# Performance work log

Hardware: AMD Instinct MI355X
Metric: run time of the kernel (lower is better)

## Reference

```python
import jax, jax.numpy as jnp
import numpy as np

N_NODES = 100000
N_EDGES = 1600000
IN_C = 128
HID_C = 128
OUT_C = 64
N_GRAPHS = 64


def setup_inputs() -> dict:
    key = jax.random.key(0)
    ks = jax.random.split(key, 12)
    x = jax.random.normal(ks[0], (N_NODES, IN_C), dtype=jnp.float32)
    edge_index = jax.random.randint(ks[1], (2, N_EDGES), 0, N_NODES, dtype=jnp.int64)
    batch = jnp.sort(jax.random.randint(ks[2], (N_NODES,), 0, N_GRAPHS, dtype=jnp.int64))
    def glorot(k, fan_in, fan_out):
        s = jnp.sqrt(6.0 / (fan_in + fan_out))
        return jax.random.uniform(k, (fan_in, fan_out), jnp.float32, -s, s)
    W1 = glorot(ks[3], IN_C, HID_C);  b1 = jnp.zeros((HID_C,), jnp.float32)
    W2 = glorot(ks[4], HID_C, HID_C); b2 = jnp.zeros((HID_C,), jnp.float32)
    W3 = glorot(ks[5], HID_C, HID_C); b3 = jnp.zeros((HID_C,), jnp.float32)
    Wlin = glorot(ks[6], HID_C, OUT_C)
    blin = jnp.zeros((OUT_C,), jnp.float32)
    return {"x": x, "edge_index": edge_index, "batch": batch,
            "W1": W1, "b1": b1, "W2": W2, "b2": b2, "W3": W3, "b3": b3,
            "Wlin": Wlin, "blin": blin}


def _gcn_conv(x, W, b, src, dst, norm):
    # PyG GCNConv: h = x @ W; out[dst] += norm * h[src]; out += b
    h = x @ W
    msg = h[src] * norm[:, None]                     # [E+N, C] edge-wise gather (memory-bound)
    out = jax.ops.segment_sum(msg, dst, num_segments=N_NODES)
    return out + b


def reference(x, edge_index, batch, W1, b1, W2, b2, W3, b3, Wlin, blin):
    # add self-loops (PyG default add_self_loops=True)
    loops = jnp.arange(N_NODES, dtype=edge_index.dtype)
    src = jnp.concatenate([edge_index[0], loops])
    dst = jnp.concatenate([edge_index[1], loops])
    # symmetric normalization: deg over dst with unit edge weights
    deg = jax.ops.segment_sum(jnp.ones_like(src, dtype=x.dtype), dst, num_segments=N_NODES)
    dinv = jnp.where(deg > 0, jax.lax.rsqrt(deg), 0.0)
    norm = dinv[src] * dinv[dst]                     # [E+N]

    h = jax.nn.relu(_gcn_conv(x, W1, b1, src, dst, norm))
    h = jax.nn.relu(_gcn_conv(h, W2, b2, src, dst, norm))
    h = jax.nn.relu(_gcn_conv(h, W3, b3, src, dst, norm))

    # global mean pool over graphs
    sums = jax.ops.segment_sum(h, batch, num_segments=N_GRAPHS)
    cnts = jax.ops.segment_sum(jnp.ones((N_NODES,), h.dtype), batch, num_segments=N_GRAPHS)
    pooled = sums / jnp.clip(cnts, 1.0)[:, None]     # [G, HID_C]
    return pooled @ Wlin + blin                      # [G, OUT_C]
```

## Files before the change

### kernel.cpp

```cpp
#include <hip/hip_runtime.h>
#include <stdint.h>

#define C_HID 128
#define NGRAPH 64
#define COUT 64
#define POOL_S 64
#define NBLK 256
#define BKT 256
#define NBUK_MAX 512
#define SCAN_CH 4096

typedef short bf16x8 __attribute__((ext_vector_type(8)));
typedef float f32x4 __attribute__((ext_vector_type(4)));
typedef float f32x2 __attribute__((ext_vector_type(2)));

__device__ __forceinline__ unsigned short f2bf(float f){
  unsigned int u = __builtin_bit_cast(unsigned int, f);
  u = u + 0x7FFFu + ((u >> 16) & 1u);
  return (unsigned short)(u >> 16);
}
__device__ __forceinline__ float bflo(unsigned int u){
  return __builtin_bit_cast(float, u << 16);
}
__device__ __forceinline__ float bfhi(unsigned int u){
  return __builtin_bit_cast(float, u & 0xFFFF0000u);
}
__device__ __forceinline__ int clampi(int v, int lo, int hi){
  return v < lo ? lo : (v > hi ? hi : v);
}

__global__ void k_zero(float* __restrict__ out, int n){
  int i = blockIdx.x*blockDim.x + threadIdx.x;
  if (i < n) out[i] = 0.f;
}

__global__ __launch_bounds__(256) void k_cnt(const int* __restrict__ dst,
                                             int* __restrict__ cntg,
                                             int E, int N, int NBUK, int chunk){
  __shared__ int cnt[NBUK_MAX];
  int blk = blockIdx.x, t = threadIdx.x;
  for (int b = t; b < NBUK; b += 256) cnt[b] = 0;
  __syncthreads();
  int e0 = blk*chunk, e1 = min(E, e0 + chunk);
  for (int e = e0 + t; e < e1; e += 256)
    atomicAdd(&cnt[clampi(dst[e], 0, N-1) >> 8], 1);
  __syncthreads();
  for (int b = t; b < NBUK; b += 256)
    cntg[b*NBLK + blk] = cnt[b];
}

__global__ __launch_bounds__(256) void k_scanA(const int* __restrict__ cnt,
                                               int* __restrict__ bsum, int n){
  __shared__ int red[256];
  int blk = blockIdx.x, t = threadIdx.x;
  int base = blk*SCAN_CH + t*16;
  int s = 0;
  #pragma unroll
  for (int j = 0; j < 16; ++j){ int i = base + j; s += (i < n) ? cnt[i] : 0; }
  red[t] = s; __syncthreads();
  for (int off = 128; off > 0; off >>= 1){
    if (t < off) red[t] += red[t + off];
    __syncthreads();
  }
  if (t == 0) bsum[blk] = red[0];
}

__global__ __launch_bounds__(256) void k_scanB(const int* __restrict__ bsum,
                                               int* __restrict__ bbase,
                                               int* __restrict__ bases, int nb, int n){
  __shared__ int buf[256];
  int t = threadIdx.x;
  int v = (t < nb) ? bsum[t] : 0;
  buf[t] = v; __syncthreads();
  for (int off = 1; off < 256; off <<= 1){
    int add = (t >= off) ? buf[t-off] : 0;
    __syncthreads();
    buf[t] += add;
    __syncthreads();
  }
  if (t < nb) bbase[t] = buf[t] - v;
  if (t == nb-1) bases[n] = buf[t];
}

__global__ __launch_bounds__(256) void k_scanC(const int* __restrict__ cnt,
                                               const int* __restrict__ bbase,
                                               int* __restrict__ bases, int n){
  __shared__ int buf[256];
  int blk = blockIdx.x, t = threadIdx.x;
  int base = blk*SCAN_CH + t*16;
  int loc[16]; int s = 0;
  #pragma unroll
  for (int j = 0; j < 16; ++j){ int i = base + j; loc[j] = (i < n) ? cnt[i] : 0; s += loc[j]; }
  buf[t] = s; __syncthreads();
  for (int off = 1; off < 256; off <<= 1){
    int add = (t >= off) ? buf[t-off] : 0;
    __syncthreads();
    buf[t] += add;
    __syncthreads();
  }
  int run = bbase[blk] + buf[t] - s;
  #pragma unroll
  for (int j = 0; j < 16; ++j){
    int i = base + j;
    if (i < n) bases[i] = run;
    run += loc[j];
  }
}

__global__ __launch_bounds__(256) void k_scat(const int* __restrict__ src,
                                              const int* __restrict__ dst,
                                              const int* __restrict__ bases,
                                              unsigned int* __restrict__ rec,
                                              int E, int N, int NBUK, int chunk){
  __shared__ int cur[NBUK_MAX];
  int blk = blockIdx.x, t = threadIdx.x;
  for (int b = t; b < NBUK; b += 256) cur[b] = bases[b*NBLK + blk];
  __syncthreads();
  int e0 = blk*chunk, e1 = min(E, e0 + chunk);
  for (int e = e0 + t; e < e1; e += 256){
    int d = clampi(dst[e], 0, N-1);
    int s = clampi(src[e], 0, N-1);
    int p = atomicAdd(&cur[d >> 8], 1);
    rec[p] = (unsigned int)s | ((unsigned int)(d & 255) << 24);
  }
}

__global__ __launch_bounds__(256) void k_csr(const unsigned int* __restrict__ rec,
                                             const int* __restrict__ bases,
                                             int* __restrict__ offs, float* __restrict__ dinv,
                                             int* __restrict__ meta, int E, int N, int NBUK){
  __shared__ int cnt[BKT], loff[BKT], cur[BKT];
  int b = blockIdx.x, t = threadIdx.x;
  cnt[t] = 0;
  __syncthreads();
  int r0 = bases[b*NBLK];
  int r1 = (b+1 < NBUK) ? bases[(b+1)*NBLK] : E;
  for (int i = r0 + t; i < r1; i += 256)
    atomicAdd(&cnt[rec[i] >> 24], 1);
  __syncthreads();
  loff[t] = cnt[t];
  __syncthreads();
  for (int off = 1; off < BKT; off <<= 1){
    int add = (t >= off) ? loff[t - off] : 0;
    __syncthreads();
    loff[t] += add;
    __syncthreads();
  }
  int excl = loff[t] - cnt[t];
  cur[t] = r0 + excl;
  int node = b*BKT + t;
  if (node < N){
    offs[node] = r0 + excl;
    dinv[node] = rsqrtf((float)(cnt[t] + 1));
  }
  if (b == NBUK-1 && t == 0) offs[N] = E;
  __syncthreads();
  for (int i = r0 + t; i < r1; i += 256){
    unsigned int r = rec[i];
    int p = atomicAdd(&cur[r >> 24], 1);
    meta[p] = (int)(r & 0x00FFFFFFu);
  }
}

__global__ void k_xcast(const float2* __restrict__ x, const float* __restrict__ dinv,
                        unsigned short* __restrict__ y, unsigned short* __restrict__ y2, int N){
  int i = blockIdx.x*256 + threadIdx.x;
  int tot = N*64;
  if (i < tot){
    float2 v = x[i];
    float dn = dinv[i >> 6] * 64.f;
    int p = __builtin_amdgcn_cvt_pk_fp8_f32(v.x*dn, v.y*dn, 0, false);
    y[i] = (unsigned short)(p & 0xFFFF);
  } else if (i < tot + 64){
    y[i] = 0;
    y2[i] = 0;
  }
}

__global__ void k_prep(const float* __restrict__ W1, const float* __restrict__ W2,
                       const float* __restrict__ W3, unsigned short* __restrict__ Wt){
  int idx = blockIdx.x*256 + threadIdx.x;
  int w = idx >> 14;
  int r = idx & 16383;
  int n = r & 127, k = r >> 7;
  const float* W = (w == 0) ? W1 : (w == 1) ? W2 : W3;
  Wt[(size_t)w*16384 + (size_t)n*128 + k] = f2bf(W[k*128 + n]);
}

__global__ void k_spmm(const unsigned short* __restrict__ y, const int* __restrict__ offs,
                       const float* __restrict__ dinv, const int* __restrict__ meta,
                       unsigned int* __restrict__ agg, int N){
  int wv   = __builtin_amdgcn_readfirstlane(threadIdx.x >> 6);
  int lane = threadIdx.x & 63;
  int node = blockIdx.x*4 + wv;
  if (node >= N) return;
  int e0 = offs[node], e1 = offs[node+1];
  int cnt = e1 - e0;
  const int* mrow = meta + e0;

  float ax, ay;
  { f32x2 f = __builtin_amdgcn_cvt_pk_f32_fp8((int)y[(size_t)node*64 + lane], false);
    ax = f.x; ay = f.y; }

  for (int e = 0; e < cnt; e += 8){
    int s[8]; unsigned short u[8];
    #pragma unroll
    for (int j = 0; j < 8; ++j){
      int ij = e + j;
      int sj = mrow[ij];
      s[j] = (ij < cnt) ? sj : N;
    }
    #pragma unroll
    for (int j = 0; j < 8; ++j)
      u[j] = y[(size_t)s[j]*64 + lane];
    #pragma unroll
    for (int j = 0; j < 8; ++j){
      f32x2 f = __builtin_amdgcn_cvt_pk_f32_fp8((int)u[j], false);
      ax += f.x;
      ay += f.y;
    }
  }
  float dn = dinv[node] * 0.015625f;
  ax *= dn; ay *= dn;
  agg[(size_t)node*64 + lane] = (unsigned int)f2bf(ax) | ((unsigned int)f2bf(ay) << 16);
}

#define GEMM_BLOCKS 512
template<bool FP8OUT>
__global__ __launch_bounds__(256) void k_gemm(const unsigned short* __restrict__ A,
                                              const unsigned short* __restrict__ Wt,
                                              const float* __restrict__ bias,
                                              const float* __restrict__ scale,
                                              void* __restrict__ outv, int M){
  __shared__ unsigned short wt[128*136];
  {
    const uint4* wsrc = (const uint4*)Wt;
    for (int i = threadIdx.x; i < 4096; i += 256){
      uint4 v = wsrc[i];
      int n = i >> 4, kblk = i & 15;
      *(uint4*)&wt[n*136 + kblk*8] = v;
    }
  }
  __syncthreads();

  int wv = threadIdx.x >> 6, lane = threadIdx.x & 63;
  int q = lane >> 4, ln = lane & 15;
  int tiles = (M + 63) >> 6;

  for (int tile = blockIdx.x; tile < tiles; tile += GEMM_BLOCKS){
    int m0 = tile*64 + wv*16;
    int arow = m0 + ln;
    bool arow_ok = (arow < M);
    int arow_s = arow_ok ? arow : 0;

    f32x4 zero = {0.f, 0.f, 0.f, 0.f};
    f32x4 acc[8];
    #pragma unroll
    for (int t = 0; t < 8; ++t) acc[t] = zero;

    #pragma unroll
    for (int kk = 0; kk < 4; ++kk){
      bf16x8 a;
      if (arow_ok){
        __builtin_memcpy(&a, A + (size_t)arow_s*128 + kk*32 + q*8, 16);
      } else {
        a = (bf16x8){0,0,0,0,0,0,0,0};
      }
      #pragma unroll
      for (int t = 0; t < 8; ++t){
        bf16x8 b;
        __builtin_memcpy(&b, &wt[(t*16 + ln)*136 + kk*32 + q*8], 16);
        acc[t] = __builtin_amdgcn_mfma_f32_16x16x32_bf16(a, b, acc[t], 0, 0, 0);
      }
    }
    float sc[4];
    #pragma unroll
    for (int r = 0; r < 4; ++r){
      int row = m0 + q*4 + r;
      sc[r] = (FP8OUT && row < M) ? scale[row] * 64.f : 1.0f;
    }
    #pragma unroll
    for (int t = 0; t < 8; ++t){
      float bv = bias[t*16 + ln];
      #pragma unroll
      for (int r = 0; r < 4; ++r){
        int row = m0 + q*4 + r;
        if (row < M){
          float v = acc[t][r] + bv;
          v = v > 0.f ? v : 0.f;
          if (FP8OUT){
            v *= sc[r];
            int p = __builtin_amdgcn_cvt_pk_fp8_f32(v, v, 0, false);
            ((unsigned char*)outv)[(size_t)row*128 + t*16 + ln] = (unsigned char)(p & 0xFF);
          } else {
            ((unsigned short*)outv)[(size_t)row*128 + t*16 + ln] = f2bf(v);
          }
        }
      }
    }
  }
}

__device__ __forceinline__ int lower_bound_i(const int* arr, int n, int val){
  int lo = 0, hi = n;
  while (lo < hi){ int mid = (lo + hi) >> 1; if (arr[mid] < val) lo = mid + 1; else hi = mid; }
  return lo;
}

__global__ void k_pool(const unsigned int* __restrict__ x, const int* __restrict__ batch,
                       float* __restrict__ partial, int N){
  int g = blockIdx.x / POOL_S, s = blockIdx.x % POOL_S;
  int h = threadIdx.x >> 6;
  int lane = threadIdx.x & 63;
  int rs = clampi(lower_bound_i(batch, N, g), 0, N);
  int re = clampi(lower_bound_i(batch, N, g + 1), rs, N);
  int len = re - rs;
  int a = rs + (int)(((long long)len * s) / POOL_S);
  int b = rs + (int)(((long long)len * (s + 1)) / POOL_S);
  float ax = 0.f, ay = 0.f;
  for (int i = a + h; i < b; i += 2){
    unsigned int u = x[(size_t)i*64 + lane];
    ax += bflo(u);
    ay += bfhi(u);
  }
  float* p = partial + ((size_t)(g*POOL_S + s)*2 + h)*C_HID;
  p[2*lane]   = ax;
  p[2*lane+1] = ay;
}

__global__ void k_final(const float* __restrict__ partial, const int* __restrict__ batch,
                        const float* __restrict__ Wl, const float* __restrict__ bl,
                        float* __restrict__ out, int N){
  __shared__ float sums[C_HID];
  int g = blockIdx.x;
  int t = threadIdx.x;
  float acc = 0.f;
  const float* p = partial + (size_t)g*POOL_S*2*C_HID;
  for (int j = 0; j < POOL_S*2; ++j)
    acc += p[j*C_HID + t];
  sums[t] = acc;
  __syncthreads();
  if (t < COUT){
    int rs = clampi(lower_bound_i(batch, N, g), 0, N);
    int re = clampi(lower_bound_i(batch, N, g + 1), rs, N);
    float inv = 1.0f / fmaxf((float)(re - rs), 1.0f);
    float o = 0.f;
    for (int k = 0; k < 128; ++k)
      o += sums[k] * Wl[k*COUT + t];
    out[g*COUT + t] = o * inv + bl[t];
  }
}

extern "C" void kernel_launch(void* const* d_in, const int* in_sizes, int n_in,
                              void* d_out, int out_size, void* d_ws, size_t ws_size,
                              hipStream_t stream){
  const float* x0 = (const float*)d_in[0];
  const int* ei   = (const int*)d_in[1];
  const int* batch= (const int*)d_in[2];
  const float* W1 = (const float*)d_in[3];
  const float* b1 = (const float*)d_in[4];
  const float* W2 = (const float*)d_in[5];
  const float* b2 = (const float*)d_in[6];
  const float* W3 = (const float*)d_in[7];
  const float* b3 = (const float*)d_in[8];
  const float* Wl = (const float*)d_in[9];
  const float* bl = (const float*)d_in[10];
  float* out = (float*)d_out;

  int E = in_sizes[1] / 2;
  int N = in_sizes[2];
  const int* src = ei;
  const int* dst = ei + E;
  int NBUK = (N + BKT - 1) / BKT;
  int chunk = (E + NBLK - 1) / NBLK;
  int ncnt = NBUK * NBLK;
  int nsb  = (ncnt + SCAN_CH - 1) / SCAN_CH;

  size_t off_acc = 0;
  auto carve = [&](size_t bytes)->size_t{
    size_t r = off_acc; off_acc += (bytes + 255) & ~(size_t)255; return r;
  };
  size_t o_cnt   = carve((size_t)ncnt*4);
  size_t o_bases = carve((size_t)(ncnt+1)*4);
  size_t o_bsum  = carve(256*4);
  size_t o_bbase = carve(256*4);
  size_t o_offs  = carve((size_t)(N+1)*4);
  size_t o_dinv  = carve((size_t)N*4);
  size_t o_meta  = carve((size_t)E*4);
  size_t o_rec   = carve((size_t)E*4);
  size_t o_yA    = carve((size_t)(N+1)*C_HID);
  size_t o_yB    = carve((size_t)(N+1)*C_HID);
  size_t o_aggb  = carve((size_t)N*C_HID*2);
  size_t o_wt    = carve((size_t)3*128*128*2);
  size_t need = off_acc;

  size_t hbuf_avail = o_aggb - o_meta;
  bool alias_ok = hbuf_avail >= (size_t)N*C_HID*2;
  alias_ok = alias_ok &&
             ((size_t)(N+1)*C_HID >= (size_t)NGRAPH*POOL_S*2*C_HID*4);

  if (ws_size < need || NBUK > NBUK_MAX || nsb > 256 || !alias_ok){
    k_zero<<<(out_size+255)/256, 256, 0, stream>>>(out, out_size);
    return;
  }

  char* base = (char*)d_ws;
  int* cntg  = (int*)(base + o_cnt);
  int* bases = (int*)(base + o_bases);
  int* bsum  = (int*)(base + o_bsum);
  int* bbase = (int*)(base + o_bbase);
  int* offs  = (int*)(base + o_offs);
  float* dinv= (float*)(base + o_dinv);
  int* meta  = (int*)(base + o_meta);
  unsigned int* rec   = (unsigned int*)(base + o_rec);
  unsigned short* yA  = (unsigned short*)(base + o_yA);
  unsigned short* yB  = (unsigned short*)(base + o_yB);
  unsigned int* aggb  = (unsigned int*)(base + o_aggb);
  unsigned short* wt  = (unsigned short*)(base + o_wt);
  unsigned short* hbuf= (unsigned short*)(base + o_meta);
  float* part         = (float*)(base + o_yB);

  k_cnt  <<<NBLK, 256, 0, stream>>>(dst, cntg, E, N, NBUK, chunk);
  k_scanA<<<nsb, 256, 0, stream>>>(cntg, bsum, ncnt);
  k_scanB<<<1, 256, 0, stream>>>(bsum, bbase, bases, nsb, ncnt);
  k_scanC<<<nsb, 256, 0, stream>>>(cntg, bbase, bases, ncnt);
  k_scat <<<NBLK, 256, 0, stream>>>(src, dst, bases, rec, E, N, NBUK, chunk);
  k_csr  <<<NBUK, BKT, 0, stream>>>(rec, bases, offs, dinv, meta, E, N, NBUK);

  k_xcast<<<(N*64 + 64 + 255)/256, 256, 0, stream>>>((const float2*)x0, dinv, yA, yB, N);
  k_prep <<<192, 256, 0, stream>>>(W1, W2, W3, wt);

  int spmm_grid = (N + 3) / 4;

  k_spmm<<<spmm_grid, 256, 0, stream>>>(yA, offs, dinv, meta, aggb, N);
  k_gemm<true ><<<GEMM_BLOCKS, 256, 0, stream>>>((const unsigned short*)aggb, wt,           b1, dinv, (void*)yB, N);
  k_spmm<<<spmm_grid, 256, 0, stream>>>(yB, offs, dinv, meta, aggb, N);
  k_gemm<true ><<<GEMM_BLOCKS, 256, 0, stream>>>((const unsigned short*)aggb, wt + 16384,   b2, dinv, (void*)yA, N);
  k_spmm<<<spmm_grid, 256, 0, stream>>>(yA, offs, dinv, meta, aggb, N);
  k_gemm<false><<<GEMM_BLOCKS, 256, 0, stream>>>((const unsigned short*)aggb, wt + 2*16384, b3, dinv, (void*)hbuf, N);

  k_pool <<<NGRAPH*POOL_S, 128, 0, stream>>>((const unsigned int*)hbuf, batch, part, N);
  k_final<<<NGRAPH, 128, 0, stream>>>(part, batch, Wl, bl, out, N);
}
```

Measured before the change: 373.6 us.

## Split wavefront into four edge groups with 8-byte gathers in SpMM

The SpMM kernel now loads all neighbor indices for a node in one coalesced read and broadcasts them with shuffles. Each wavefront is split into four 16-lane groups, and each group gathers an 8-byte fp8 chunk of a different neighbor row, so up to 32 neighbors are issued as independent loads before any accumulation. Partial sums are then reduced across groups with xor shuffles, and one group writes a 16-byte output. This is meant to cut the number of gather instructions and the dependent load latency. In exchange it adds cross-lane reduction work and a slower tail loop for nodes with more than 31 neighbors.

Result: slower. 387.8 us (+3.8%).

```diff
diff --git a/kernel.cpp b/kernel.cpp
--- a/kernel.cpp
+++ b/kernel.cpp
@@ -187,42 +187,81 @@
   Wt[(size_t)w*16384 + (size_t)n*128 + k] = f2bf(W[k*128 + n]);
 }
 
-__global__ void k_spmm(const unsigned short* __restrict__ y, const int* __restrict__ offs,
-                       const float* __restrict__ dinv, const int* __restrict__ meta,
+__global__ __launch_bounds__(256) void k_spmm(const unsigned short* __restrict__ y,
+                       const int* __restrict__ offs,
+                       const float* __restrict__ dinv,
+                       const int* __restrict__ meta,
                        unsigned int* __restrict__ agg, int N){
   int wv   = __builtin_amdgcn_readfirstlane(threadIdx.x >> 6);
   int lane = threadIdx.x & 63;
   int node = blockIdx.x*4 + wv;
   if (node >= N) return;
+  int g = lane >> 4;
+  int c = lane & 15;
+
   int e0 = offs[node], e1 = offs[node+1];
   int cnt = e1 - e0;
-  const int* mrow = meta + e0;
-
-  float ax, ay;
-  { f32x2 f = __builtin_amdgcn_cvt_pk_f32_fp8((int)y[(size_t)node*64 + lane], false);
-    ax = f.x; ay = f.y; }
-
-  for (int e = 0; e < cnt; e += 8){
-    int s[8]; unsigned short u[8];
-    #pragma unroll
-    for (int j = 0; j < 8; ++j){
-      int ij = e + j;
-      int sj = mrow[ij];
-      s[j] = (ij < cnt) ? sj : N;
-    }
-    #pragma unroll
-    for (int j = 0; j < 8; ++j)
-      u[j] = y[(size_t)s[j]*64 + lane];
-    #pragma unroll
-    for (int j = 0; j < 8; ++j){
-      f32x2 f = __builtin_amdgcn_cvt_pk_f32_fp8((int)u[j], false);
-      ax += f.x;
-      ay += f.y;
-    }
+  int mv = (lane < cnt) ? meta[e0 + lane] : N;
+
+  const uint2* yrow = (const uint2*)y;
+
+  f32x2 acc[4];
+  #pragma unroll
+  for (int k = 0; k < 4; ++k) acc[k] = (f32x2){0.f, 0.f};
+
+  int nslot = cnt + 1;
+  int ninstr = (nslot + 3) >> 2;
+  if (ninstr > 8) ninstr = 8;
+
+  uint2 u[8];
+  #pragma unroll
+  for (int k = 0; k < 8; ++k){
+    if (k < ninstr){
+      int slot = k*4 + g;
+      int idx  = slot - 1;
+      int idxc = idx < 0 ? 0 : idx;
+      int sj = __shfl(mv, idxc, 64);
+      if (slot == 0) sj = node;
+      u[k] = yrow[(size_t)sj*16 + c];
+    }
+  }
+  __builtin_amdgcn_sched_barrier(0);
+  #pragma unroll
+  for (int k = 0; k < 8; ++k){
+    if (k < ninstr){
+      f32x2 f;
+      f = __builtin_amdgcn_cvt_pk_f32_fp8((int)u[k].x, false); acc[0] += f;
+      f = __builtin_amdgcn_cvt_pk_f32_fp8((int)u[k].x, true);  acc[1] += f;
+      f = __builtin_amdgcn_cvt_pk_f32_fp8((int)u[k].y, false); acc[2] += f;
+      f = __builtin_amdgcn_cvt_pk_f32_fp8((int)u[k].y, true);  acc[3] += f;
+    }
+  }
+  for (int base = 32; base < nslot; base += 4){
+    int idx = base + g - 1;
+    int sj = (idx < cnt) ? meta[e0 + idx] : N;
+    uint2 t = yrow[(size_t)sj*16 + c];
+    f32x2 f;
+    f = __builtin_amdgcn_cvt_pk_f32_fp8((int)t.x, false); acc[0] += f;
+    f = __builtin_amdgcn_cvt_pk_f32_fp8((int)t.x, true);  acc[1] += f;
+    f = __builtin_amdgcn_cvt_pk_f32_fp8((int)t.y, false); acc[2] += f;
+    f = __builtin_amdgcn_cvt_pk_f32_fp8((int)t.y, true);  acc[3] += f;
+  }
+  #pragma unroll
+  for (int k = 0; k < 4; ++k){
+    acc[k].x += __shfl_xor(acc[k].x, 16, 64);
+    acc[k].y += __shfl_xor(acc[k].y, 16, 64);
+    acc[k].x += __shfl_xor(acc[k].x, 32, 64);
+    acc[k].y += __shfl_xor(acc[k].y, 32, 64);
   }
   float dn = dinv[node] * 0.015625f;
-  ax *= dn; ay *= dn;
-  agg[(size_t)node*64 + lane] = (unsigned int)f2bf(ax) | ((unsigned int)f2bf(ay) << 16);
+  if (g == 0){
+    uint4 w;
+    w.x = (unsigned int)f2bf(acc[0].x*dn) | ((unsigned int)f2bf(acc[0].y*dn) << 16);
+    w.y = (unsigned int)f2bf(acc[1].x*dn) | ((unsigned int)f2bf(acc[1].y*dn) << 16);
+    w.z = (unsigned int)f2bf(acc[2].x*dn) | ((unsigned int)f2bf(acc[2].y*dn) << 16);
+    w.w = (unsigned int)f2bf(acc[3].x*dn) | ((unsigned int)f2bf(acc[3].y*dn) << 16);
+    *(uint4*)(agg + (size_t)node*64 + c*4) = w;
+  }
 }
 
 #define GEMM_BLOCKS 512
```
